# Optimization experiments

Measured on AMD Instinct MI355X. Metric: run time of the kernel, lower is better.

The kernel has to match this reference:

```python
import jax, jax.numpy as jnp
import numpy as np

N_NODES = 50000
N_EDGES = 800000
IN_DIM = 256
N_HEADS = 4
HEAD_DIM = 64
NEG_SLOPE = 0.2  # PyG GATConv default


def setup_inputs() -> dict:
    key = jax.random.key(0)
    k1, k2, k3, k4, k5 = jax.random.split(key, 5)
    x = jax.random.normal(k1, (N_NODES, IN_DIM), dtype=jnp.float32)
    edge_index = jax.random.randint(k2, (2, N_EDGES), 0, N_NODES, dtype=jnp.int64)
    # Glorot-style scaling for the linear projection and attention vectors
    w_scale = (2.0 / (IN_DIM + N_HEADS * HEAD_DIM)) ** 0.5
    W = jax.random.normal(k3, (IN_DIM, N_HEADS * HEAD_DIM), dtype=jnp.float32) * w_scale
    a_scale = (2.0 / (1 + HEAD_DIM)) ** 0.5
    att_src = jax.random.normal(k4, (N_HEADS, HEAD_DIM), dtype=jnp.float32) * a_scale
    att_dst = jax.random.normal(k5, (N_HEADS, HEAD_DIM), dtype=jnp.float32) * a_scale
    return {"x": x, "edge_index": edge_index, "W": W, "att_src": att_src, "att_dst": att_dst}


def _gat_conv(x, edge_index, W, att_src, att_dst):
    n = x.shape[0]
    # PyG GATConv default: add self-loops
    loops = jnp.arange(n, dtype=edge_index.dtype)
    src = jnp.concatenate([edge_index[0], loops])  # [E+N]
    dst = jnp.concatenate([edge_index[1], loops])  # [E+N]

    xp = (x @ W).reshape(n, N_HEADS, HEAD_DIM)            # [N, H, C]
    a_src = jnp.einsum('nhc,hc->nh', xp, att_src)          # [N, H]
    a_dst = jnp.einsum('nhc,hc->nh', xp, att_dst)          # [N, H]

    e = jax.nn.leaky_relu(a_src[src] + a_dst[dst], NEG_SLOPE)  # [E+N, H]
    # segment softmax over incoming edges of each destination node
    e_max = jax.ops.segment_max(e, dst, num_segments=n)       # [N, H]
    e_exp = jnp.exp(e - e_max[dst])
    denom = jax.ops.segment_sum(e_exp, dst, num_segments=n)   # [N, H]
    alpha = e_exp / denom[dst]                                 # [E+N, H]

    # weighted scatter-aggregate of source features (concat heads, no bias)
    out = jax.ops.segment_sum(alpha[:, :, None] * xp[src], dst, num_segments=n)  # [N, H, C]
    return out.reshape(n, N_HEADS * HEAD_DIM)


def reference(x, edge_index, W, att_src, att_dst):
    y = _gat_conv(x, edge_index, W, att_src, att_dst)
    return jax.nn.relu(y)  # BackboneNet applies ReLU after each GAT block
```

## Files before the change

kernel.cpp:

```cpp
#include <hip/hip_runtime.h>
#include <hip/hip_bf16.h>

#define IN_DIM 256
#define OUT_DIM 256
#define NHEADS 4
#define NEG_SLOPE 0.2f
#define ELLW 48
#define OVFCAP (1 << 18)

typedef unsigned short u16;
typedef __attribute__((ext_vector_type(8))) short short8;
typedef __attribute__((ext_vector_type(4))) float f32x4;

__device__ __forceinline__ float bf2f(u16 v) {
    return __uint_as_float(((unsigned int)v) << 16);
}
__device__ __forceinline__ u16 f2bf(float f) {
    unsigned int b = __float_as_uint(f);
    b += 0x7FFFu + ((b >> 16) & 1u);
    return (u16)(b >> 16);
}
__device__ __forceinline__ float4 bf4(uint2 p) {
    float4 r;
    r.x = __uint_as_float(p.x << 16);
    r.y = __uint_as_float(p.x & 0xFFFF0000u);
    r.z = __uint_as_float(p.y << 16);
    r.w = __uint_as_float(p.y & 0xFFFF0000u);
    return r;
}
__device__ __forceinline__ float lrelu(float v) { return v > 0.f ? v : NEG_SLOPE * v; }

__device__ __forceinline__ int detectbf(const void* x) {
    int lane = threadIdx.x & 63;
    u16 v = ((const u16*)x)[2 * lane];
    int e = (v >> 7) & 0xFF;
    int sane = (e >= 118 && e <= 137) || ((v & 0x7FFFu) == 0);
    return __popcll(__ballot(sane)) >= 48;
}
__device__ __forceinline__ int detect64(const void* eidx) {
    int lane = threadIdx.x & 63;
    return __ballot(((const int*)eidx)[2 * lane + 1] == 0) == ~0ull;
}

__device__ __forceinline__ void eread(const void* e, int is64, int i, int E, int& s, int& d) {
    if (is64) {
        const long long* p = (const long long*)e;
        s = (int)p[i]; d = (int)p[(size_t)E + i];
    } else {
        const int* p = (const int*)e;
        s = p[i]; d = p[(size_t)E + i];
    }
}

__global__ __launch_bounds__(256) void k_conv(const void* x, const void* W,
                                              const void* as, const void* ad,
                                              u16* Wtb, float* asf, float* adf) {
    int b = blockIdx.x, t = threadIdx.x;
    int isb = detectbf(x);
    if (b == 0) {
        asf[t] = isb ? bf2f(((const u16*)as)[t]) : ((const float*)as)[t];
        adf[t] = isb ? bf2f(((const u16*)ad)[t]) : ((const float*)ad)[t];
    } else {
        int base = (b - 1) * 512;
#pragma unroll
        for (int j = 0; j < 2; ++j) {
            int i = base + t + j * 256;
            int nOut = i >> 8, k = i & 255;
            float w = isb ? bf2f(((const u16*)W)[(size_t)k * OUT_DIM + nOut])
                          : ((const float*)W)[(size_t)k * OUT_DIM + nOut];
            Wtb[i] = f2bf(w);
        }
    }
}

__global__ __launch_bounds__(256, 2) void k_main(const void* __restrict__ x,
                                                 const void* __restrict__ eidx,
                                                 const u16* __restrict__ Wtb,
                                                 const float* __restrict__ asf,
                                                 const float* __restrict__ adf,
                                                 u16* __restrict__ xpb,
                                                 float* __restrict__ a_src,
                                                 float* __restrict__ a_dst,
                                                 int* __restrict__ cnt,
                                                 int* __restrict__ ell,
                                                 int* __restrict__ ovf,
                                                 int n, int E, int ngemm) {
    if ((int)blockIdx.x < ngemm) {
        __shared__ u16 As[128][32];
        __shared__ u16 Bs[256][32];
        const int isb = detectbf(x);
        const int t = threadIdx.x;
        const int row0 = blockIdx.x * 128;
        const int wave = t >> 6, lane = t & 63;
        const int q = lane >> 4, l16 = lane & 15;
        const int wm = (wave >> 1) * 64, wn = (wave & 1) * 128;
        f32x4 acc[4][8];
#pragma unroll
        for (int a = 0; a < 4; ++a)
#pragma unroll
            for (int b = 0; b < 8; ++b) acc[a][b] = (f32x4){0.f, 0.f, 0.f, 0.f};

        const int sr = t >> 3;
        const int sk = (t & 7) * 4;

        for (int k0 = 0; k0 < IN_DIM; k0 += 32) {
#pragma unroll
            for (int i = 0; i < 4; ++i) {
                int rr = sr + i * 32;
                int grow = row0 + rr; if (grow >= n) grow = n - 1;
                uint2 pk;
                if (isb) {
                    pk = *(const uint2*)((const u16*)x + (size_t)grow * IN_DIM + k0 + sk);
                } else {
                    const float* xf = (const float*)x + (size_t)grow * IN_DIM + k0 + sk;
                    float4 v = *(const float4*)xf;
                    pk.x = ((unsigned)f2bf(v.y) << 16) | f2bf(v.x);
                    pk.y = ((unsigned)f2bf(v.w) << 16) | f2bf(v.z);
                }
                *(uint2*)&As[rr][sk] = pk;
            }
#pragma unroll
            for (int i = 0; i < 8; ++i) {
                int rr = sr + i * 32;
                *(uint2*)&Bs[rr][sk] = *(const uint2*)(Wtb + (size_t)rr * IN_DIM + k0 + sk);
            }
            __syncthreads();
            short8 af[4], bfr[8];
#pragma unroll
            for (int mt = 0; mt < 4; ++mt)
                af[mt] = *(const short8*)&As[wm + mt * 16 + l16][q * 8];
#pragma unroll
            for (int nt = 0; nt < 8; ++nt)
                bfr[nt] = *(const short8*)&Bs[wn + nt * 16 + l16][q * 8];
#pragma unroll
            for (int mt = 0; mt < 4; ++mt)
#pragma unroll
                for (int nt = 0; nt < 8; ++nt)
                    acc[mt][nt] = __builtin_amdgcn_mfma_f32_16x16x32_bf16(
                        af[mt], bfr[nt], acc[mt][nt], 0, 0, 0);
            __syncthreads();
        }
#pragma unroll
        for (int mt = 0; mt < 4; ++mt) {
#pragma unroll
            for (int nt = 0; nt < 8; ++nt) {
                int col = wn + nt * 16 + l16;
#pragma unroll
                for (int r = 0; r < 4; ++r) {
                    int row = row0 + wm + mt * 16 + q * 4 + r;
                    if (row < n) xpb[(size_t)row * OUT_DIM + col] = f2bf(acc[mt][nt][r]);
                }
            }
        }
        float asv[8], adv[8];
#pragma unroll
        for (int nt = 0; nt < 8; ++nt) {
            int col = wn + nt * 16 + l16;
            asv[nt] = asf[col]; adv[nt] = adf[col];
        }
        int h0 = wn >> 6;
#pragma unroll
        for (int mt = 0; mt < 4; ++mt) {
#pragma unroll
            for (int r = 0; r < 4; ++r) {
                float vs0 = acc[mt][0][r] * asv[0] + acc[mt][1][r] * asv[1]
                          + acc[mt][2][r] * asv[2] + acc[mt][3][r] * asv[3];
                float vd0 = acc[mt][0][r] * adv[0] + acc[mt][1][r] * adv[1]
                          + acc[mt][2][r] * adv[2] + acc[mt][3][r] * adv[3];
                float vs1 = acc[mt][4][r] * asv[4] + acc[mt][5][r] * asv[5]
                          + acc[mt][6][r] * asv[6] + acc[mt][7][r] * asv[7];
                float vd1 = acc[mt][4][r] * adv[4] + acc[mt][5][r] * adv[5]
                          + acc[mt][6][r] * adv[6] + acc[mt][7][r] * adv[7];
#pragma unroll
                for (int m = 1; m < 16; m <<= 1) {
                    vs0 += __shfl_xor(vs0, m); vd0 += __shfl_xor(vd0, m);
                    vs1 += __shfl_xor(vs1, m); vd1 += __shfl_xor(vd1, m);
                }
                if (l16 == 0) {
                    int row = row0 + wm + mt * 16 + q * 4 + r;
                    if (row < n) {
                        a_src[row * NHEADS + h0] = vs0;
                        a_dst[row * NHEADS + h0] = vd0;
                        a_src[row * NHEADS + h0 + 1] = vs1;
                        a_dst[row * NHEADS + h0 + 1] = vd1;
                    }
                }
            }
        }
    } else {
        const int is64 = detect64(eidx);
        int i = ((int)blockIdx.x - ngemm) * 256 + threadIdx.x;
        if (i < E) {
            int s, d;
            eread(eidx, is64, i, E, s, d);
            int pos = atomicAdd(&cnt[d], 1);
            if (pos < ELLW) {
                ell[d * ELLW + pos] = s;
            } else {
                int o = atomicAdd(&cnt[n], 1) & (OVFCAP - 1);
                ovf[2 * o] = d; ovf[2 * o + 1] = s;
            }
        }
    }
}

__global__ __launch_bounds__(256) void k_agg(const int* __restrict__ cnt,
                                             const int* __restrict__ ell,
                                             const int* __restrict__ ovf,
                                             const float* __restrict__ a_src,
                                             const float* __restrict__ a_dst,
                                             const u16* __restrict__ xpb,
                                             void* out, const void* x, int n) {
    int isb = detectbf(x);
    int d = (blockIdx.x * 256 + threadIdx.x) >> 6;
    int lane = threadIdx.x & 63;
    if (d >= n) return;
    int h = lane >> 4;
    int deg = cnt[d];
    int m = deg < ELLW ? deg : ELLW;
    const int* row = ell + d * ELLW;
    float ad = a_dst[d * NHEADS + h];
    float vsf = fminf(lrelu(a_src[d * NHEADS + h] + ad), 80.f);
    float wsf = __expf(vsf);
    float4 xs = bf4(((const uint2*)(xpb + (size_t)d * OUT_DIM))[lane]);
    float4 acc;
    acc.x = wsf * xs.x; acc.y = wsf * xs.y; acc.z = wsf * xs.z; acc.w = wsf * xs.w;
    float den = wsf;
    int e = 0;
    for (; e + 8 <= m; e += 8) {
        int s[8]; uint2 p[8]; float w[8];
#pragma unroll
        for (int j = 0; j < 8; ++j) s[j] = row[e + j];
#pragma unroll
        for (int j = 0; j < 8; ++j)
            p[j] = ((const uint2*)(xpb + (size_t)s[j] * OUT_DIM))[lane];
#pragma unroll
        for (int j = 0; j < 8; ++j) {
            float v = fminf(lrelu(a_src[s[j] * NHEADS + h] + ad), 80.f);
            w[j] = __expf(v);
        }
#pragma unroll
        for (int j = 0; j < 8; ++j) {
            float4 xv = bf4(p[j]);
            acc.x += w[j] * xv.x; acc.y += w[j] * xv.y;
            acc.z += w[j] * xv.z; acc.w += w[j] * xv.w;
            den += w[j];
        }
    }
    for (; e < m; ++e) {
        int s = row[e];
        float v = fminf(lrelu(a_src[s * NHEADS + h] + ad), 80.f);
        float w = __expf(v);
        float4 xv = bf4(((const uint2*)(xpb + (size_t)s * OUT_DIM))[lane]);
        acc.x += w * xv.x; acc.y += w * xv.y; acc.z += w * xv.z; acc.w += w * xv.w;
        den += w;
    }
    if (deg > ELLW) {
        int movf = cnt[n]; if (movf > OVFCAP) movf = OVFCAP;
        for (int i = 0; i < movf; ++i) {
            if (ovf[2 * i] == d) {
                int s = ovf[2 * i + 1];
                float v = fminf(lrelu(a_src[s * NHEADS + h] + ad), 80.f);
                float w = __expf(v);
                float4 xv = bf4(((const uint2*)(xpb + (size_t)s * OUT_DIM))[lane]);
                acc.x += w * xv.x; acc.y += w * xv.y; acc.z += w * xv.z; acc.w += w * xv.w;
                den += w;
            }
        }
    }
    float rd = 1.f / den;
    float o0 = fmaxf(acc.x * rd, 0.f);
    float o1 = fmaxf(acc.y * rd, 0.f);
    float o2 = fmaxf(acc.z * rd, 0.f);
    float o3 = fmaxf(acc.w * rd, 0.f);
    size_t idx = (size_t)d * OUT_DIM + lane * 4;
    if (isb) {
        u16 p4[4] = {f2bf(o0), f2bf(o1), f2bf(o2), f2bf(o3)};
        *(uint2*)((u16*)out + idx) = *(const uint2*)p4;
    } else {
        float p4[4] = {o0, o1, o2, o3};
        *(float4*)((float*)out + idx) = *(const float4*)p4;
    }
}

extern "C" void kernel_launch(void* const* d_in, const int* in_sizes, int n_in,
                              void* d_out, int out_size, void* d_ws, size_t ws_size,
                              hipStream_t stream) {
    const void* x    = d_in[0];
    const void* eidx = d_in[1];
    const void* W    = d_in[2];
    const void* as   = d_in[3];
    const void* ad   = d_in[4];
    int n = in_sizes[0] / IN_DIM;
    int E = in_sizes[1] / 2;

    char* ws = (char*)d_ws;
    size_t off_b = 0;
    auto alloc = [&](size_t bytes) -> void* {
        void* p = ws + off_b;
        off_b += (bytes + 255) & ~(size_t)255;
        return p;
    };
    u16*   Wtb    = (u16*)alloc((size_t)IN_DIM * OUT_DIM * 2);
    float* asf    = (float*)alloc(256 * 4);
    float* adf    = (float*)alloc(256 * 4);
    u16*   xpb    = (u16*)alloc((size_t)n * OUT_DIM * 2);
    float* a_src  = (float*)alloc((size_t)n * NHEADS * 4);
    float* a_dst  = (float*)alloc((size_t)n * NHEADS * 4);
    int*   cnt    = (int*)alloc((size_t)(n + 1) * 4);
    int*   ell    = (int*)alloc((size_t)n * ELLW * 4);
    int*   ovf    = (int*)alloc((size_t)OVFCAP * 8);

    int ngemm = (n + 127) / 128;
    int nell  = (E + 255) / 256;

    hipMemsetAsync(cnt, 0, (size_t)(n + 1) * 4, stream);

    hipLaunchKernelGGL(k_conv, dim3(129), dim3(256), 0, stream,
                       x, W, as, ad, Wtb, asf, adf);
    hipLaunchKernelGGL(k_main, dim3(ngemm + nell), dim3(256), 0, stream,
                       x, eidx, Wtb, asf, adf, xpb, a_src, a_dst, cnt, ell, ovf, n, E, ngemm);
    hipLaunchKernelGGL(k_agg, dim3((n + 3) / 4), dim3(256), 0, stream,
                       cnt, ell, ovf, a_src, a_dst, xpb, d_out, x, n);
}
```

Before: 244.1 us.

## Move edge ELL bucketing into prep kernel, split GEMM into its own kernel

The edge-to-ELL scatter blocks move from the combined GEMM/edge kernel into the weight-conversion prep kernel, and the projection GEMM becomes a standalone kernel. The aim is to keep the atomic-heavy edge scatter from sharing a launch with the register-heavy MFMA GEMM (launch bounds 256,2), so the GEMM runs at uniform occupancy and the scatter overlaps with the tiny weight conversion. The cost is that the edge work no longer overlaps with the GEMM, so the total may become more serial.

```diff
diff --git a/kernel.cpp b/kernel.cpp
--- a/kernel.cpp
+++ b/kernel.cpp
@@ -52,15 +52,17 @@
     }
 }
 
-__global__ __launch_bounds__(256) void k_conv(const void* x, const void* W,
-                                              const void* as, const void* ad,
-                                              u16* Wtb, float* asf, float* adf) {
+__global__ __launch_bounds__(256) void k_prep(const void* x, const void* eidx,
+                                              const void* W, const void* as, const void* ad,
+                                              u16* Wtb, float* asf, float* adf,
+                                              int* cnt, int* ell, int* ovf, int n, int E) {
     int b = blockIdx.x, t = threadIdx.x;
-    int isb = detectbf(x);
     if (b == 0) {
+        int isb = detectbf(x);
         asf[t] = isb ? bf2f(((const u16*)as)[t]) : ((const float*)as)[t];
         adf[t] = isb ? bf2f(((const u16*)ad)[t]) : ((const float*)ad)[t];
-    } else {
+    } else if (b <= 128) {
+        int isb = detectbf(x);
         int base = (b - 1) * 512;
 #pragma unroll
         for (int j = 0; j < 2; ++j) {
@@ -70,126 +72,9 @@
                           : ((const float*)W)[(size_t)k * OUT_DIM + nOut];
             Wtb[i] = f2bf(w);
         }
-    }
-}
-
-__global__ __launch_bounds__(256, 2) void k_main(const void* __restrict__ x,
-                                                 const void* __restrict__ eidx,
-                                                 const u16* __restrict__ Wtb,
-                                                 const float* __restrict__ asf,
-                                                 const float* __restrict__ adf,
-                                                 u16* __restrict__ xpb,
-                                                 float* __restrict__ a_src,
-                                                 float* __restrict__ a_dst,
-                                                 int* __restrict__ cnt,
-                                                 int* __restrict__ ell,
-                                                 int* __restrict__ ovf,
-                                                 int n, int E, int ngemm) {
-    if ((int)blockIdx.x < ngemm) {
-        __shared__ u16 As[128][32];
-        __shared__ u16 Bs[256][32];
-        const int isb = detectbf(x);
-        const int t = threadIdx.x;
-        const int row0 = blockIdx.x * 128;
-        const int wave = t >> 6, lane = t & 63;
-        const int q = lane >> 4, l16 = lane & 15;
-        const int wm = (wave >> 1) * 64, wn = (wave & 1) * 128;
-        f32x4 acc[4][8];
-#pragma unroll
-        for (int a = 0; a < 4; ++a)
-#pragma unroll
-            for (int b = 0; b < 8; ++b) acc[a][b] = (f32x4){0.f, 0.f, 0.f, 0.f};
-
-        const int sr = t >> 3;
-        const int sk = (t & 7) * 4;
-
-        for (int k0 = 0; k0 < IN_DIM; k0 += 32) {
-#pragma unroll
-            for (int i = 0; i < 4; ++i) {
-                int rr = sr + i * 32;
-                int grow = row0 + rr; if (grow >= n) grow = n - 1;
-                uint2 pk;
-                if (isb) {
-                    pk = *(const uint2*)((const u16*)x + (size_t)grow * IN_DIM + k0 + sk);
-                } else {
-                    const float* xf = (const float*)x + (size_t)grow * IN_DIM + k0 + sk;
-                    float4 v = *(const float4*)xf;
-                    pk.x = ((unsigned)f2bf(v.y) << 16) | f2bf(v.x);
-                    pk.y = ((unsigned)f2bf(v.w) << 16) | f2bf(v.z);
-                }
-                *(uint2*)&As[rr][sk] = pk;
-            }
-#pragma unroll
-            for (int i = 0; i < 8; ++i) {
-                int rr = sr + i * 32;
-                *(uint2*)&Bs[rr][sk] = *(const uint2*)(Wtb + (size_t)rr * IN_DIM + k0 + sk);
-            }
-            __syncthreads();
-            short8 af[4], bfr[8];
-#pragma unroll
-            for (int mt = 0; mt < 4; ++mt)
-                af[mt] = *(const short8*)&As[wm + mt * 16 + l16][q * 8];
-#pragma unroll
-            for (int nt = 0; nt < 8; ++nt)
-                bfr[nt] = *(const short8*)&Bs[wn + nt * 16 + l16][q * 8];
-#pragma unroll
-            for (int mt = 0; mt < 4; ++mt)
-#pragma unroll
-                for (int nt = 0; nt < 8; ++nt)
-                    acc[mt][nt] = __builtin_amdgcn_mfma_f32_16x16x32_bf16(
-                        af[mt], bfr[nt], acc[mt][nt], 0, 0, 0);
-            __syncthreads();
-        }
-#pragma unroll
-        for (int mt = 0; mt < 4; ++mt) {
-#pragma unroll
-            for (int nt = 0; nt < 8; ++nt) {
-                int col = wn + nt * 16 + l16;
-#pragma unroll
-                for (int r = 0; r < 4; ++r) {
-                    int row = row0 + wm + mt * 16 + q * 4 + r;
-                    if (row < n) xpb[(size_t)row * OUT_DIM + col] = f2bf(acc[mt][nt][r]);
-                }
-            }
-        }
-        float asv[8], adv[8];
-#pragma unroll
-        for (int nt = 0; nt < 8; ++nt) {
-            int col = wn + nt * 16 + l16;
-            asv[nt] = asf[col]; adv[nt] = adf[col];
-        }
-        int h0 = wn >> 6;
-#pragma unroll
-        for (int mt = 0; mt < 4; ++mt) {
-#pragma unroll
-            for (int r = 0; r < 4; ++r) {
-                float vs0 = acc[mt][0][r] * asv[0] + acc[mt][1][r] * asv[1]
-                          + acc[mt][2][r] * asv[2] + acc[mt][3][r] * asv[3];
-                float vd0 = acc[mt][0][r] * adv[0] + acc[mt][1][r] * adv[1]
-                          + acc[mt][2][r] * adv[2] + acc[mt][3][r] * adv[3];
-                float vs1 = acc[mt][4][r] * asv[4] + acc[mt][5][r] * asv[5]
-                          + acc[mt][6][r] * asv[6] + acc[mt][7][r] * asv[7];
-                float vd1 = acc[mt][4][r] * adv[4] + acc[mt][5][r] * adv[5]
-                          + acc[mt][6][r] * adv[6] + acc[mt][7][r] * adv[7];
-#pragma unroll
-                for (int m = 1; m < 16; m <<= 1) {
-                    vs0 += __shfl_xor(vs0, m); vd0 += __shfl_xor(vd0, m);
-                    vs1 += __shfl_xor(vs1, m); vd1 += __shfl_xor(vd1, m);
-                }
-                if (l16 == 0) {
-                    int row = row0 + wm + mt * 16 + q * 4 + r;
-                    if (row < n) {
-                        a_src[row * NHEADS + h0] = vs0;
-                        a_dst[row * NHEADS + h0] = vd0;
-                        a_src[row * NHEADS + h0 + 1] = vs1;
-                        a_dst[row * NHEADS + h0 + 1] = vd1;
-                    }
-                }
-            }
-        }
     } else {
         const int is64 = detect64(eidx);
-        int i = ((int)blockIdx.x - ngemm) * 256 + threadIdx.x;
+        int i = (b - 129) * 256 + t;
         if (i < E) {
             int s, d;
             eread(eidx, is64, i, E, s, d);
@@ -199,6 +84,116 @@
             } else {
                 int o = atomicAdd(&cnt[n], 1) & (OVFCAP - 1);
                 ovf[2 * o] = d; ovf[2 * o + 1] = s;
+            }
+        }
+    }
+}
+
+__global__ __launch_bounds__(256, 2) void k_gemm(const void* __restrict__ x,
+                                                 const u16* __restrict__ Wtb,
+                                                 const float* __restrict__ asf,
+                                                 const float* __restrict__ adf,
+                                                 u16* __restrict__ xpb,
+                                                 float* __restrict__ a_src,
+                                                 float* __restrict__ a_dst, int n) {
+    __shared__ u16 As[128][32];
+    __shared__ u16 Bs[256][32];
+    const int isb = detectbf(x);
+    const int t = threadIdx.x;
+    const int row0 = blockIdx.x * 128;
+    const int wave = t >> 6, lane = t & 63;
+    const int q = lane >> 4, l16 = lane & 15;
+    const int wm = (wave >> 1) * 64, wn = (wave & 1) * 128;
+    f32x4 acc[4][8];
+#pragma unroll
+    for (int a = 0; a < 4; ++a)
+#pragma unroll
+        for (int b = 0; b < 8; ++b) acc[a][b] = (f32x4){0.f, 0.f, 0.f, 0.f};
+
+    const int sr = t >> 3;
+    const int sk = (t & 7) * 4;
+
+    for (int k0 = 0; k0 < IN_DIM; k0 += 32) {
+#pragma unroll
+        for (int i = 0; i < 4; ++i) {
+            int rr = sr + i * 32;
+            int grow = row0 + rr; if (grow >= n) grow = n - 1;
+            uint2 pk;
+            if (isb) {
+                pk = *(const uint2*)((const u16*)x + (size_t)grow * IN_DIM + k0 + sk);
+            } else {
+                const float* xf = (const float*)x + (size_t)grow * IN_DIM + k0 + sk;
+                float4 v = *(const float4*)xf;
+                pk.x = ((unsigned)f2bf(v.y) << 16) | f2bf(v.x);
+                pk.y = ((unsigned)f2bf(v.w) << 16) | f2bf(v.z);
+            }
+            *(uint2*)&As[rr][sk] = pk;
+        }
+#pragma unroll
+        for (int i = 0; i < 8; ++i) {
+            int rr = sr + i * 32;
+            *(uint2*)&Bs[rr][sk] = *(const uint2*)(Wtb + (size_t)rr * IN_DIM + k0 + sk);
+        }
+        __syncthreads();
+        short8 af[4], bfr[8];
+#pragma unroll
+        for (int mt = 0; mt < 4; ++mt)
+            af[mt] = *(const short8*)&As[wm + mt * 16 + l16][q * 8];
+#pragma unroll
+        for (int nt = 0; nt < 8; ++nt)
+            bfr[nt] = *(const short8*)&Bs[wn + nt * 16 + l16][q * 8];
+#pragma unroll
+        for (int mt = 0; mt < 4; ++mt)
+#pragma unroll
+            for (int nt = 0; nt < 8; ++nt)
+                acc[mt][nt] = __builtin_amdgcn_mfma_f32_16x16x32_bf16(
+                    af[mt], bfr[nt], acc[mt][nt], 0, 0, 0);
+        __syncthreads();
+    }
+#pragma unroll
+    for (int mt = 0; mt < 4; ++mt) {
+#pragma unroll
+        for (int nt = 0; nt < 8; ++nt) {
+            int col = wn + nt * 16 + l16;
+#pragma unroll
+            for (int r = 0; r < 4; ++r) {
+                int row = row0 + wm + mt * 16 + q * 4 + r;
+                if (row < n) xpb[(size_t)row * OUT_DIM + col] = f2bf(acc[mt][nt][r]);
+            }
+        }
+    }
+    float asv[8], adv[8];
+#pragma unroll
+    for (int nt = 0; nt < 8; ++nt) {
+        int col = wn + nt * 16 + l16;
+        asv[nt] = asf[col]; adv[nt] = adf[col];
+    }
+    int h0 = wn >> 6;
+#pragma unroll
+    for (int mt = 0; mt < 4; ++mt) {
+#pragma unroll
+        for (int r = 0; r < 4; ++r) {
+            float vs0 = acc[mt][0][r] * asv[0] + acc[mt][1][r] * asv[1]
+                      + acc[mt][2][r] * asv[2] + acc[mt][3][r] * asv[3];
+            float vd0 = acc[mt][0][r] * adv[0] + acc[mt][1][r] * adv[1]
+                      + acc[mt][2][r] * adv[2] + acc[mt][3][r] * adv[3];
+            float vs1 = acc[mt][4][r] * asv[4] + acc[mt][5][r] * asv[5]
+                      + acc[mt][6][r] * asv[6] + acc[mt][7][r] * asv[7];
+            float vd1 = acc[mt][4][r] * adv[4] + acc[mt][5][r] * adv[5]
+                      + acc[mt][6][r] * adv[6] + acc[mt][7][r] * adv[7];
+#pragma unroll
+            for (int m = 1; m < 16; m <<= 1) {
+                vs0 += __shfl_xor(vs0, m); vd0 += __shfl_xor(vd0, m);
+                vs1 += __shfl_xor(vs1, m); vd1 += __shfl_xor(vd1, m);
+            }
+            if (l16 == 0) {
+                int row = row0 + wm + mt * 16 + q * 4 + r;
+                if (row < n) {
+                    a_src[row * NHEADS + h0] = vs0;
+                    a_dst[row * NHEADS + h0] = vd0;
+                    a_src[row * NHEADS + h0 + 1] = vs1;
+                    a_dst[row * NHEADS + h0 + 1] = vd1;
+                }
             }
         }
     }
@@ -316,10 +311,10 @@
 
     hipMemsetAsync(cnt, 0, (size_t)(n + 1) * 4, stream);
 
-    hipLaunchKernelGGL(k_conv, dim3(129), dim3(256), 0, stream,
-                       x, W, as, ad, Wtb, asf, adf);
-    hipLaunchKernelGGL(k_main, dim3(ngemm + nell), dim3(256), 0, stream,
-                       x, eidx, Wtb, asf, adf, xpb, a_src, a_dst, cnt, ell, ovf, n, E, ngemm);
+    hipLaunchKernelGGL(k_prep, dim3(129 + nell), dim3(256), 0, stream,
+                       x, eidx, W, as, ad, Wtb, asf, adf, cnt, ell, ovf, n, E);
+    hipLaunchKernelGGL(k_gemm, dim3(ngemm), dim3(256), 0, stream,
+                       x, Wtb, asf, adf, xpb, a_src, a_dst, n);
     hipLaunchKernelGGL(k_agg, dim3((n + 3) / 4), dim3(256), 0, stream,
                        cnt, ell, ovf, a_src, a_dst, xpb, d_out, x, n);
 }
```

Result: slower. 259.4 us (+6.2%).
